# Optimization experiments

Hardware: AMD Instinct MI355X
Metric: run time of the kernel (lower is better)

Reference implementation:

```python
import jax, jax.numpy as jnp
import numpy as np
from jax import lax

C = 384
B, H, W = 16, 56, 56
EPS = 1e-5
KS = [5, 7, 7, 3, 3, 3]
DIL = [1, 1, 2, 3, 4, 5]


def _dwconv(x, w, dilation):
    # depthwise conv, groups == channels; SAME-style padding (r*(k-1)+1)//2
    k = w.shape[-1]
    p = (dilation * (k - 1) + 1) // 2
    return lax.conv_general_dilated(
        x, w, window_strides=(1, 1), padding=[(p, p), (p, p)],
        rhs_dilation=(dilation, dilation),
        dimension_numbers=('NCHW', 'OIHW', 'NCHW'),
        feature_group_count=x.shape[1])


def _bn(x, p):
    # inference-mode BatchNorm2d: p = [gamma, beta, running_mean, running_var], each [C]
    g, b, m, v = p[0], p[1], p[2], p[3]
    scale = (g * lax.rsqrt(v + EPS)).reshape(1, -1, 1, 1)
    shift = (b - m * g * lax.rsqrt(v + EPS)).reshape(1, -1, 1, 1)
    return x * scale + shift


def setup_inputs() -> dict:
    key = jax.random.key(0)
    ks = jax.random.split(key, 10)
    inp = {
        'x': jax.random.normal(ks[0], (B, C, H, W), jnp.float32),
        'lk_w': jax.random.normal(ks[1], (C, 1, 13, 13), jnp.float32) * 0.05,
        'obn': jax.random.uniform(ks[2], (4, C), jnp.float32),
        'w5': jax.random.normal(ks[3], (C, 1, 5, 5), jnp.float32) * 0.05,
        'w7a': jax.random.normal(ks[4], (C, 1, 7, 7), jnp.float32) * 0.05,
        'w7b': jax.random.normal(ks[5], (C, 1, 7, 7), jnp.float32) * 0.05,
        'w3a': jax.random.normal(ks[6], (C, 1, 3, 3), jnp.float32) * 0.05,
        'w3b': jax.random.normal(ks[7], (C, 1, 3, 3), jnp.float32) * 0.05,
        'w3c': jax.random.normal(ks[8], (C, 1, 3, 3), jnp.float32) * 0.05,
        'br_bn': jax.random.uniform(ks[9], (6, 4, C), jnp.float32),
    }
    return inp


def reference(x, lk_w, obn, w5, w7a, w7b, w3a, w3b, w3c, br_bn):
    out = _bn(_dwconv(x, lk_w, 1), obn)  # origin 13x13 branch
    ws = [w5, w7a, w7b, w3a, w3b, w3c]
    for i, (w, r) in enumerate(zip(ws, DIL)):
        out = out + _bn(_dwconv(x, w, r), br_bn[i])
    return out
```

## Files before the change

kernel.cpp:

```cpp
#include <hip/hip_runtime.h>
#include <hip/hip_bf16.h>

#define C_ 384
#define B_ 16
#define H_ 56
#define W_ 56
#define WROW_ 8
#define SPSZ_ 4944

typedef _Float16 f16x8 __attribute__((ext_vector_type(8)));
typedef float    f32x4 __attribute__((ext_vector_type(4)));

__device__ __forceinline__ float foldw(int c, int py, int px,
    const float* lk, const float* w5, const float* w7a, const float* w7b,
    const float* w3a, const float* w3b, const float* w3c, const float* sc)
{
    int dy = py - 6, dx = px - 6;
    float a = sc[0] * lk[c * 169 + py * 13 + px];
#define ADDBR(Wp, K, R, SI)                                               \
    {                                                                     \
        const int half = ((K) - 1) / 2;                                   \
        if (dy % (R) == 0 && dx % (R) == 0) {                             \
            int iy = dy / (R), ix = dx / (R);                             \
            if (iy >= -half && iy <= half && ix >= -half && ix <= half)   \
                a += sc[SI] * Wp[c * (K) * (K) + (iy + half) * (K) + (ix + half)]; \
        }                                                                 \
    }
    ADDBR(w5,  5, 1, 1)
    ADDBR(w7a, 7, 1, 2)
    ADDBR(w7b, 7, 2, 3)
    ADDBR(w3a, 3, 3, 4)
    ADDBR(w3b, 3, 4, 5)
    ADDBR(w3c, 3, 5, 6)
#undef ADDBR
    return a;
}

__global__ void build_weights_kernel(
    const float* __restrict__ lk, const float* __restrict__ obn,
    const float* __restrict__ w5, const float* __restrict__ w7a,
    const float* __restrict__ w7b, const float* __restrict__ w3a,
    const float* __restrict__ w3b, const float* __restrict__ w3c,
    const float* __restrict__ brbn,
    unsigned* __restrict__ wpk, float* __restrict__ bias)
{
    int c = blockIdx.x;
    int t = threadIdx.x;

    float sc[7], sh[7];
    {
        float g = obn[c], b = obn[C_ + c], m = obn[2 * C_ + c], v = obn[3 * C_ + c];
        float s = g * rsqrtf(v + 1e-5f);
        sc[0] = s; sh[0] = b - m * s;
    }
#pragma unroll
    for (int i = 0; i < 6; ++i) {
        float g = brbn[(i * 4 + 0) * C_ + c], b = brbn[(i * 4 + 1) * C_ + c];
        float m = brbn[(i * 4 + 2) * C_ + c], v = brbn[(i * 4 + 3) * C_ + c];
        float s = g * rsqrtf(v + 1e-5f);
        sc[i + 1] = s; sh[i + 1] = b - m * s;
    }

    if (t < 13 * WROW_) {
        int ky = t / WROW_, pp = t % WROW_;
        int kx0 = 2 * pp, kx1 = 2 * pp + 1;
        float w0 = (kx0 < 13) ? foldw(c, ky, kx0, lk, w5, w7a, w7b, w3a, w3b, w3c, sc) : 0.f;
        float w1 = (kx1 < 13) ? foldw(c, ky, kx1, lk, w5, w7a, w7b, w3a, w3b, w3c, sc) : 0.f;
        _Float16 h0 = (_Float16)w0, h1 = (_Float16)w1;
        unsigned u = ((unsigned)__builtin_bit_cast(unsigned short, h1) << 16)
                   |  (unsigned)__builtin_bit_cast(unsigned short, h0);
        wpk[c * 13 * WROW_ + t] = u;
    }
    if (t == 0) {
        float s = 0.f;
#pragma unroll
        for (int i = 0; i < 7; ++i) s += sh[i];
        bias[c] = s;
    }
}

__global__ __launch_bounds__(256, 3) void dwconv13_mfma(
    const float* __restrict__ x, const unsigned* __restrict__ wpk,
    const float* __restrict__ bias, float* __restrict__ out)
{
    __shared__ unsigned sPd[2][SPSZ_];
    __shared__ unsigned sQ[320];

    const int bid = blockIdx.x;
    const int c   = bid % C_;
    const int q   = bid / C_;
    const int t   = threadIdx.x;

    int dd[13];
    unsigned vv[13];

#define STAGE_ISSUE(b0v)                                                    \
    {                                                                       \
        _Pragma("unroll")                                                   \
        for (int k = 0; k < 13; ++k) {                                      \
            int slot = t + k * 256;                                         \
            if (k < 12 || slot < 3136) {                                    \
                int p  = slot / 1568, rem = slot - p * 1568;                \
                int iy = rem / 28,    pr  = rem - iy * 28;                  \
                const float* xp = x + ((size_t)(((b0v) + p) * C_ + c)) * (H_ * W_); \
                float2 v = *(const float2*)(xp + iy * W_ + pr * 2);         \
                _Float16 h0 = (_Float16)v.x, h1 = (_Float16)v.y;            \
                vv[k] = ((unsigned)__builtin_bit_cast(unsigned short, h1) << 16) \
                      |  (unsigned)__builtin_bit_cast(unsigned short, h0);  \
            }                                                               \
        }                                                                   \
    }

#pragma unroll
    for (int k = 0; k < 13; ++k) {
        int slot = t + k * 256;
        if (k < 12 || slot < 3136) {
            int p  = slot / 1568, rem = slot - p * 1568;
            int iy = rem / 28,    pr  = rem - iy * 28;
            dd[k] = p * 2448 + (iy + 6) * 36 + 3 + pr;
        } else dd[k] = 0;
    }

    STAGE_ISSUE(4 * q)
#pragma unroll
    for (int k = 0; k < 2; ++k) {
        int s = t + k * 256;
        if (s < 320) {
            unsigned qv = 0;
            if (s < 312) {
                int ky = s / 24, t24 = s - ky * 24;
                if (t24 >= 8 && t24 < 16) qv = wpk[c * 104 + ky * 8 + (t24 - 8)];
            }
            sQ[s] = qv;
        }
    }
    {
        uint4 z = make_uint4(0u, 0u, 0u, 0u);
        uint4* s4 = (uint4*)&sPd[0][0];
        const int tot4 = (2 * SPSZ_) / 4;
#pragma unroll
        for (int k = 0; k < 10; ++k) {
            int slot = t + k * 256;
            if (k < 9 || slot < tot4) s4[slot] = z;
        }
    }
    __syncthreads();

#pragma unroll
    for (int k = 0; k < 13; ++k) {
        int slot = t + k * 256;
        if (k < 12 || slot < 3136) sPd[0][dd[k]] = vv[k];
    }
    __syncthreads();

    const float bv  = bias[c];
    const int lane = t & 63;
    const int wv   = t >> 6;
    const int x0   = wv * 16;
    const int g    = lane >> 4, n = lane & 15;
    const int r8   = lane & 7,  pp = (lane >> 3) & 1;

    const int q0 = 16 + 8 * g - n;
    const int v0 = q0 >> 1;
    const unsigned shb = (unsigned)(q0 & 1) * 16u;
    f16x8 bf[13];
#pragma unroll
    for (int ky = 0; ky < 13; ++ky) {
        const unsigned* Q = sQ + ky * 24 + v0;
        unsigned U0 = Q[0], U1 = Q[1], U2 = Q[2], U3 = Q[3], U4 = Q[4];
        uint4 u;
        u.x = __builtin_amdgcn_alignbit(U1, U0, shb);
        u.y = __builtin_amdgcn_alignbit(U2, U1, shb);
        u.z = __builtin_amdgcn_alignbit(U3, U2, shb);
        u.w = __builtin_amdgcn_alignbit(U4, U3, shb);
        bf[ky] = __builtin_bit_cast(f16x8, u);
    }

    const int aBase = pp * 2448 + r8 * 36 + x0 / 2 + 4 * g;
    const int xo = x0 + n;

#define COMPUTE(BUF, b0v)                                                   \
    {                                                                       \
        const unsigned* sp = &sPd[BUF][0];                                  \
        _Pragma("unroll")                                                   \
        for (int ty = 0; ty < 7; ++ty) {                                    \
            f32x4 d0 = { bv, bv, bv, bv };                                  \
            f32x4 d1 = { 0.f, 0.f, 0.f, 0.f };                              \
            int base = aBase + (8 * ty) * 36;                               \
            uint4 ua = *(const uint4*)(sp + base);                          \
            _Pragma("unroll")                                               \
            for (int ky = 0; ky < 13; ++ky) {                               \
                uint4 un;                                                   \
                if (ky < 12) un = *(const uint4*)(sp + base + (ky + 1) * 36); \
                f16x8 a = __builtin_bit_cast(f16x8, ua);                    \
                if (ky & 1) d1 = __builtin_amdgcn_mfma_f32_16x16x32_f16(a, bf[ky], d1, 0, 0, 0); \
                else        d0 = __builtin_amdgcn_mfma_f32_16x16x32_f16(a, bf[ky], d0, 0, 0, 0); \
                if (ky < 12) ua = un;                                       \
            }                                                               \
            d0 = d0 + d1;                                                   \
            if (xo < W_) {                                                  \
                _Pragma("unroll")                                           \
                for (int r = 0; r < 4; ++r) {                               \
                    int m  = 4 * g + r;                                     \
                    int p2 = m >> 3, rr = m & 7;                            \
                    out[((size_t)(((b0v) + p2) * C_ + c)) * (H_ * W_)       \
                        + (8 * ty + rr) * W_ + xo] = d0[r];                 \
                }                                                           \
            }                                                               \
        }                                                                   \
    }

    STAGE_ISSUE(4 * q + 2)

    COMPUTE(0, 4 * q)

#pragma unroll
    for (int k = 0; k < 13; ++k) {
        int slot = t + k * 256;
        if (k < 12 || slot < 3136) sPd[1][dd[k]] = vv[k];
    }
    __syncthreads();

    COMPUTE(1, 4 * q + 2)

#undef COMPUTE
#undef STAGE_ISSUE
}

extern "C" void kernel_launch(void* const* d_in, const int* in_sizes, int n_in,
                              void* d_out, int out_size, void* d_ws, size_t ws_size,
                              hipStream_t stream) {
    const float* x    = (const float*)d_in[0];
    const float* lk   = (const float*)d_in[1];
    const float* obn  = (const float*)d_in[2];
    const float* w5   = (const float*)d_in[3];
    const float* w7a  = (const float*)d_in[4];
    const float* w7b  = (const float*)d_in[5];
    const float* w3a  = (const float*)d_in[6];
    const float* w3b  = (const float*)d_in[7];
    const float* w3c  = (const float*)d_in[8];
    const float* brbn = (const float*)d_in[9];
    float* out  = (float*)d_out;

    unsigned* wpk  = (unsigned*)d_ws;
    float*    bias = (float*)(wpk + C_ * 13 * WROW_);

    hipLaunchKernelGGL(build_weights_kernel, dim3(C_), dim3(128), 0, stream,
                       lk, obn, w5, w7a, w7b, w3a, w3b, w3c, brbn, wpk, bias);

    hipLaunchKernelGGL(dwconv13_mfma, dim3((B_ / 4) * C_), dim3(256), 0, stream,
                       x, wpk, bias, out);
}
```

Measured before the change: 43.61 us.

## Process eight images per block with single LDS buffer and register double-buffering

Each block now handles four image pairs instead of two, halving the grid, and uses one shared-memory tile instead of two. The next pair's global loads are issued into alternating register arrays while the current pair is computed, then committed to LDS between barriers. This halves LDS use, which may raise occupancy, and spreads the weight and bias setup over more work. The cost is more barriers per block, more live registers from two staging arrays, and fewer blocks for load balancing.

```diff
diff --git a/kernel.cpp b/kernel.cpp
--- a/kernel.cpp
+++ b/kernel.cpp
@@ -83,18 +83,29 @@
     const float* __restrict__ x, const unsigned* __restrict__ wpk,
     const float* __restrict__ bias, float* __restrict__ out)
 {
-    __shared__ unsigned sPd[2][SPSZ_];
+    __shared__ unsigned sP[SPSZ_];
     __shared__ unsigned sQ[320];
 
     const int bid = blockIdx.x;
     const int c   = bid % C_;
     const int q   = bid / C_;
+    const int b0  = 8 * q;
     const int t   = threadIdx.x;
 
     int dd[13];
-    unsigned vv[13];
-
-#define STAGE_ISSUE(b0v)                                                    \
+#pragma unroll
+    for (int k = 0; k < 13; ++k) {
+        int slot = t + k * 256;
+        if (k < 12 || slot < 3136) {
+            int p  = slot / 1568, rem = slot - p * 1568;
+            int iy = rem / 28,    pr  = rem - iy * 28;
+            dd[k] = p * 2448 + (iy + 6) * 36 + 3 + pr;
+        } else dd[k] = 0;
+    }
+
+    unsigned vvA[13], vvB[13];
+
+#define STAGE_ISSUE(vv, b0v)                                                \
     {                                                                       \
         _Pragma("unroll")                                                   \
         for (int k = 0; k < 13; ++k) {                                      \
@@ -105,23 +116,22 @@
                 const float* xp = x + ((size_t)(((b0v) + p) * C_ + c)) * (H_ * W_); \
                 float2 v = *(const float2*)(xp + iy * W_ + pr * 2);         \
                 _Float16 h0 = (_Float16)v.x, h1 = (_Float16)v.y;            \
-                vv[k] = ((unsigned)__builtin_bit_cast(unsigned short, h1) << 16) \
-                      |  (unsigned)__builtin_bit_cast(unsigned short, h0);  \
+                (vv)[k] = ((unsigned)__builtin_bit_cast(unsigned short, h1) << 16) \
+                        |  (unsigned)__builtin_bit_cast(unsigned short, h0); \
             }                                                               \
         }                                                                   \
     }
 
-#pragma unroll
-    for (int k = 0; k < 13; ++k) {
-        int slot = t + k * 256;
-        if (k < 12 || slot < 3136) {
-            int p  = slot / 1568, rem = slot - p * 1568;
-            int iy = rem / 28,    pr  = rem - iy * 28;
-            dd[k] = p * 2448 + (iy + 6) * 36 + 3 + pr;
-        } else dd[k] = 0;
-    }
-
-    STAGE_ISSUE(4 * q)
+#define COMMIT(vv)                                                          \
+    {                                                                       \
+        _Pragma("unroll")                                                   \
+        for (int k = 0; k < 13; ++k) {                                      \
+            int slot = t + k * 256;                                         \
+            if (k < 12 || slot < 3136) sP[dd[k]] = (vv)[k];                 \
+        }                                                                   \
+    }
+
+    STAGE_ISSUE(vvA, b0)
 #pragma unroll
     for (int k = 0; k < 2; ++k) {
         int s = t + k * 256;
@@ -136,21 +146,15 @@
     }
     {
         uint4 z = make_uint4(0u, 0u, 0u, 0u);
-        uint4* s4 = (uint4*)&sPd[0][0];
-        const int tot4 = (2 * SPSZ_) / 4;
-#pragma unroll
-        for (int k = 0; k < 10; ++k) {
+        uint4* s4 = (uint4*)sP;
+#pragma unroll
+        for (int k = 0; k < 5; ++k) {
             int slot = t + k * 256;
-            if (k < 9 || slot < tot4) s4[slot] = z;
+            if (k < 4 || slot < SPSZ_ / 4) s4[slot] = z;
         }
     }
     __syncthreads();
-
-#pragma unroll
-    for (int k = 0; k < 13; ++k) {
-        int slot = t + k * 256;
-        if (k < 12 || slot < 3136) sPd[0][dd[k]] = vv[k];
-    }
+    COMMIT(vvA)
     __syncthreads();
 
     const float bv  = bias[c];
@@ -179,19 +183,18 @@
     const int aBase = pp * 2448 + r8 * 36 + x0 / 2 + 4 * g;
     const int xo = x0 + n;
 
-#define COMPUTE(BUF, b0v)                                                   \
+#define COMPUTE(b0v)                                                        \
     {                                                                       \
-        const unsigned* sp = &sPd[BUF][0];                                  \
         _Pragma("unroll")                                                   \
         for (int ty = 0; ty < 7; ++ty) {                                    \
             f32x4 d0 = { bv, bv, bv, bv };                                  \
             f32x4 d1 = { 0.f, 0.f, 0.f, 0.f };                              \
             int base = aBase + (8 * ty) * 36;                               \
-            uint4 ua = *(const uint4*)(sp + base);                          \
+            uint4 ua = *(const uint4*)(sP + base);                          \
             _Pragma("unroll")                                               \
             for (int ky = 0; ky < 13; ++ky) {                               \
                 uint4 un;                                                   \
-                if (ky < 12) un = *(const uint4*)(sp + base + (ky + 1) * 36); \
+                if (ky < 12) un = *(const uint4*)(sP + base + (ky + 1) * 36); \
                 f16x8 a = __builtin_bit_cast(f16x8, ua);                    \
                 if (ky & 1) d1 = __builtin_amdgcn_mfma_f32_16x16x32_f16(a, bf[ky], d1, 0, 0, 0); \
                 else        d0 = __builtin_amdgcn_mfma_f32_16x16x32_f16(a, bf[ky], d0, 0, 0, 0); \
@@ -210,20 +213,28 @@
         }                                                                   \
     }
 
-    STAGE_ISSUE(4 * q + 2)
-
-    COMPUTE(0, 4 * q)
-
-#pragma unroll
-    for (int k = 0; k < 13; ++k) {
-        int slot = t + k * 256;
-        if (k < 12 || slot < 3136) sPd[1][dd[k]] = vv[k];
-    }
-    __syncthreads();
-
-    COMPUTE(1, 4 * q + 2)
+    STAGE_ISSUE(vvB, b0 + 2)
+    COMPUTE(b0)
+    __syncthreads();
+    COMMIT(vvB)
+    __syncthreads();
+
+    STAGE_ISSUE(vvA, b0 + 4)
+    COMPUTE(b0 + 2)
+    __syncthreads();
+    COMMIT(vvA)
+    __syncthreads();
+
+    STAGE_ISSUE(vvB, b0 + 6)
+    COMPUTE(b0 + 4)
+    __syncthreads();
+    COMMIT(vvB)
+    __syncthreads();
+
+    COMPUTE(b0 + 6)
 
 #undef COMPUTE
+#undef COMMIT
 #undef STAGE_ISSUE
 }
 
@@ -248,6 +259,6 @@
     hipLaunchKernelGGL(build_weights_kernel, dim3(C_), dim3(128), 0, stream,
                        lk, obn, w5, w7a, w7b, w3a, w3b, w3c, brbn, wpk, bias);
 
-    hipLaunchKernelGGL(dwconv13_mfma, dim3((B_ / 4) * C_), dim3(256), 0, stream,
+    hipLaunchKernelGGL(dwconv13_mfma, dim3((B_ / 8) * C_), dim3(256), 0, stream,
                        x, wpk, bias, out);
 }
```

Result: slower. 59.93 us (+37.4%).
